# Optimization experiments

Measured on AMD Instinct MI355X. Metric: run time of the kernel, lower is better.

The kernel has to match this reference:

```python
import jax, jax.numpy as jnp
import numpy as np


def setup_inputs() -> dict:
    key = jax.random.key(0)
    k1, = jax.random.split(key, 1)
    B, L, D = 128, 1024, 768
    hidden_states = jax.random.normal(k1, (B, L, D), dtype=jnp.float32)
    attention_mask = jnp.zeros((B, 1, 1, L), dtype=jnp.float32)
    return {"hidden_states": hidden_states, "attention_mask": attention_mask, "K": 512}


def reference(hidden_states, attention_mask, K):
    B, L, D = hidden_states.shape
    # r tokens to merge, protected class token (ToMe: r = min(r, (t - protected)//2))
    r = max(0, L - K)
    r = min(r, (L - 1) // 2)

    # --- bipartite soft matching (indices computed under no_grad in torch) ---
    metric = hidden_states / jnp.linalg.norm(hidden_states, axis=-1, keepdims=True)
    a = metric[:, ::2, :]   # [B, t1, D] even tokens (src side)
    b = metric[:, 1::2, :]  # [B, t2, D] odd tokens (dst side)
    scores = jnp.einsum('bid,bjd->bij', a, b)  # [B, t1, t2]
    scores = scores.at[:, 0, :].set(-jnp.inf)  # protect class token (row 0 of src)
    node_max = jnp.max(scores, axis=-1)        # [B, t1]
    node_idx = jnp.argmax(scores, axis=-1)     # [B, t1] best dst per src
    order = jnp.argsort(-node_max, axis=-1)    # descending similarity
    src_idx = order[:, :r]                     # [B, r] tokens to merge away
    unm_idx = jnp.sort(order[:, r:], axis=-1)  # [B, t1-r] kept src tokens (sorted: class_token=True)
    dst_idx = jnp.take_along_axis(node_idx, src_idx, axis=-1)  # [B, r]

    # --- merge(x, mode='mean') with include_self=True ---
    src = hidden_states[:, ::2, :]   # [B, t1, D]
    dst = hidden_states[:, 1::2, :]  # [B, t2, D]
    t2 = dst.shape[1]
    unm = jnp.take_along_axis(src, unm_idx[..., None], axis=1)     # [B, t1-r, D]
    src_g = jnp.take_along_axis(src, src_idx[..., None], axis=1)   # [B, r, D]
    bidx = jnp.arange(B)[:, None]
    dst_sum = dst.at[bidx, dst_idx].add(src_g)                     # self + merged srcs
    counts = jnp.ones((B, t2), dtype=hidden_states.dtype).at[bidx, dst_idx].add(1.0)
    dst_mean = dst_sum / counts[..., None]

    preserved_tokens = jnp.concatenate([unm, dst_mean], axis=1)    # [B, t1-r+t2, D]
    final_attention_mask = jnp.zeros((B, 1, 1, preserved_tokens.shape[1]),
                                     dtype=hidden_states.dtype)
    return preserved_tokens, final_attention_mask
```

## Files before the change

### kernel.cpp

```cpp
#include <hip/hip_runtime.h>
#include <hip/hip_bf16.h>

#define B_ 128
#define L_ 1024
#define T_ 512
#define D_ 768
#define CH_ 96
#define DT_ 513
#define TAU_C 1e-3f
#define PBUF_ 1024

typedef __attribute__((ext_vector_type(8))) short bf16x8;
typedef __attribute__((ext_vector_type(4))) float f32x4;

typedef const __attribute__((address_space(1))) unsigned int* gas1_t;
typedef __attribute__((address_space(3))) unsigned int* gas3_t;

__device__ __forceinline__ unsigned short f2bf_rne(float x){
    unsigned u = __float_as_uint(x);
    unsigned r = (u + 0x7FFFu + ((u >> 16) & 1u)) >> 16;
    return (unsigned short)r;
}

__global__ __launch_bounds__(256) void pack_k(const float* __restrict__ hs,
                                              unsigned short* __restrict__ Apk,
                                              unsigned short* __restrict__ Bpk,
                                              double* __restrict__ nsq,
                                              int* __restrict__ paircnt){
    __shared__ __align__(16) unsigned short LhS[CH_ * 16 * 8];
    if (blockIdx.x == 0 && threadIdx.x == 0) *paircnt = 0;
    int b = blockIdx.x >> 6, g = blockIdx.x & 63;
    int wv = threadIdx.x >> 6, lane = threadIdx.x & 63;

    #pragma unroll
    for (int rr = 0; rr < 4; ++rr){
        int jj = wv * 4 + rr;
        long seq = (long)b * L_ + g * 16 + jj;
        const float4* src = (const float4*)(hs + seq * D_);
        float4 f0 = src[lane], f1 = src[lane + 64], f2 = src[lane + 128];
        double s = 0.0;
        s += (double)f0.x*f0.x + (double)f0.y*f0.y + (double)f0.z*f0.z + (double)f0.w*f0.w;
        s += (double)f1.x*f1.x + (double)f1.y*f1.y + (double)f1.z*f1.z + (double)f1.w*f1.w;
        s += (double)f2.x*f2.x + (double)f2.y*f2.y + (double)f2.z*f2.z + (double)f2.w*f2.w;
        #pragma unroll
        for (int off = 32; off; off >>= 1) s += __shfl_xor(s, off);
        if (lane == 0 && (jj & 1)) nsq[seq] = s;
        float rn = (float)(1.0 / sqrt(s));
        float4 fv[3] = {f0, f1, f2};
        #pragma unroll
        for (int t = 0; t < 3; ++t){
            int e0 = t * 256 + lane * 4;
            int c = e0 >> 3, ei = e0 & 7;
            float vv[4] = {fv[t].x, fv[t].y, fv[t].z, fv[t].w};
            short4 hv;
            #pragma unroll
            for (int e = 0; e < 4; ++e)
                ((short*)&hv)[e] = (short)f2bf_rne(vv[e] * rn);
            int o = c * 128 + ((jj ^ (c & 7)) << 3) + ei;
            *(short4*)(LhS + o) = hv;
        }
    }
    __syncthreads();
    #pragma unroll
    for (int it = 0; it < 6; ++it){
        int linear = it * 256 + threadIdx.x;
        int c = linear >> 4, jj = linear & 15;
        int o = c * 128 + ((jj ^ (c & 7)) << 3);
        int tok = g * 8 + (jj >> 1);
        long go = ((long)(b * CH_ + c) * T_ + tok) * 8;
        if (jj & 1) *(bf16x8*)(Bpk + go) = *(const bf16x8*)(LhS + o);
        else        *(bf16x8*)(Apk + go) = *(const bf16x8*)(LhS + o);
    }
}

__global__ __launch_bounds__(512, 2) void coarse_k(const unsigned short* __restrict__ Apk,
                                                   const unsigned short* __restrict__ Bpk,
                                                   int* __restrict__ node_idx,
                                                   unsigned long long* __restrict__ rowkey,
                                                   int* __restrict__ paircnt,
                                                   int2* __restrict__ pairs){
    __shared__ __align__(16) unsigned short A_lds[CH_ * 64 * 8];
    __shared__ float pm1s[64][8];
    __shared__ int   pjs [64][8];
    __shared__ float m1f[64];
    __shared__ int   cnd[64];
    __shared__ int2  pbuf[PBUF_];
    __shared__ int   pcnt_s, pbase_s;

    int bid = blockIdx.x;
    int xcd = bid & 7, q = bid >> 3;
    int it = q & 7, bhi = q >> 3;
    int b = xcd + 8 * bhi;

    int tid = threadIdx.x;
    int w = tid >> 6, lane = tid & 63, l15 = lane & 15, l4 = lane >> 4;

    long pkbase = (long)b * CH_ * T_;

    #pragma unroll
    for (int n = 0; n < 12; ++n){
        int c = w * 12 + n;
        const unsigned short* src = Apk + (pkbase + (long)c * T_ + it * 64 + lane) * 8;
        __builtin_amdgcn_global_load_lds((gas1_t)src, (gas3_t)(A_lds + c * 512), 16, 0, 0);
    }

    const unsigned short* pB0 = Bpk + (pkbase + (long)l4 * T_ + w * 64 + l15) * 8;
    const long KSTEP = (long)4 * T_ * 8;

    f32x4 acc[4][4];
    #pragma unroll
    for (int i = 0; i < 4; ++i)
        #pragma unroll
        for (int j = 0; j < 4; ++j) acc[i][j] = (f32x4){0.f, 0.f, 0.f, 0.f};

    bf16x8 bq0[4], bq1[4];
    #pragma unroll
    for (int jb = 0; jb < 4; ++jb){
        bq0[jb] = *(const bf16x8*)(pB0 + 0 * KSTEP + jb * 128);
        bq1[jb] = *(const bf16x8*)(pB0 + 1 * KSTEP + jb * 128);
    }
    __syncthreads();

    if (tid == 0) pcnt_s = 0;

    #pragma unroll
    for (int s = 0; s < 24; ++s){
        bf16x8 bq2[4];
        if (s < 22){
            #pragma unroll
            for (int jb = 0; jb < 4; ++jb)
                bq2[jb] = *(const bf16x8*)(pB0 + (long)(s + 2) * KSTEP + jb * 128);
        }
        bf16x8 ah[4];
        #pragma unroll
        for (int ib = 0; ib < 4; ++ib)
            ah[ib] = *(const bf16x8*)(A_lds + ((s * 4 + l4) * 64 + ib * 16 + l15) * 8);
        if (s & 1){
            #pragma unroll
            for (int jb = 0; jb < 4; ++jb)
                #pragma unroll
                for (int ib = 0; ib < 4; ++ib)
                    acc[ib][jb] = __builtin_amdgcn_mfma_f32_16x16x32_bf16(ah[ib], bq1[jb], acc[ib][jb], 0, 0, 0);
            if (s < 22){
                #pragma unroll
                for (int jb = 0; jb < 4; ++jb) bq1[jb] = bq2[jb];
            }
        } else {
            #pragma unroll
            for (int jb = 0; jb < 4; ++jb)
                #pragma unroll
                for (int ib = 0; ib < 4; ++ib)
                    acc[ib][jb] = __builtin_amdgcn_mfma_f32_16x16x32_bf16(ah[ib], bq0[jb], acc[ib][jb], 0, 0, 0);
            if (s < 22){
                #pragma unroll
                for (int jb = 0; jb < 4; ++jb) bq0[jb] = bq2[jb];
            }
        }
    }

    #pragma unroll
    for (int ib = 0; ib < 4; ++ib)
        #pragma unroll
        for (int rr = 0; rr < 4; ++rr){
            float m1 = -1e30f; int j1 = 0;
            #pragma unroll
            for (int jb = 0; jb < 4; ++jb){
                float v = acc[ib][jb][rr];
                int col = w * 64 + jb * 16 + l15;
                if (v > m1){ m1 = v; j1 = col; }
            }
            #pragma unroll
            for (int m = 1; m < 16; m <<= 1){
                float o1 = __shfl_xor(m1, m);
                int   oj = __shfl_xor(j1, m);
                if (o1 > m1 || (o1 == m1 && oj < j1)){ m1 = o1; j1 = oj; }
            }
            if (l15 == 0){
                int row = ib * 16 + l4 * 4 + rr;
                pm1s[row][w] = m1; pjs[row][w] = j1;
            }
        }
    __syncthreads();
    int grow0 = b * T_ + it * 64;
    if (tid < 64){
        float M1 = -1e30f; int J1 = 0;
        #pragma unroll
        for (int w2 = 0; w2 < 8; ++w2){
            float a1 = pm1s[tid][w2]; int aj = pjs[tid][w2];
            if (a1 > M1){ M1 = a1; J1 = aj; }
        }
        node_idx[grow0 + tid] = J1;
        m1f[tid] = M1;
        cnd[tid] = 0;
        rowkey[grow0 + tid] = 0ULL;
    }
    __syncthreads();
    #pragma unroll
    for (int ib = 0; ib < 4; ++ib)
        #pragma unroll
        for (int rr = 0; rr < 4; ++rr){
            int row = ib * 16 + l4 * 4 + rr;
            float thr_ = m1f[row] - TAU_C;
            int hits = 0;
            #pragma unroll
            for (int jb = 0; jb < 4; ++jb) hits += (acc[ib][jb][rr] > thr_) ? 1 : 0;
            if (hits) atomicAdd(&cnd[row], hits);
        }
    __syncthreads();
    #pragma unroll
    for (int ib = 0; ib < 4; ++ib)
        #pragma unroll
        for (int rr = 0; rr < 4; ++rr){
            int row = ib * 16 + l4 * 4 + rr;
            if (cnd[row] < 2) continue;
            if (it == 0 && row == 0) continue;
            float thr_ = m1f[row] - TAU_C;
            #pragma unroll
            for (int jb = 0; jb < 4; ++jb)
                if (acc[ib][jb][rr] > thr_){
                    int idx = atomicAdd(&pcnt_s, 1);
                    int2 pr = make_int2(grow0 + row, w * 64 + jb * 16 + l15);
                    if (idx < PBUF_) pbuf[idx] = pr;
                    else { int p = atomicAdd(paircnt, 1); pairs[p] = pr; }
                }
        }
    __syncthreads();
    if (tid == 0){
        int n = min(pcnt_s, PBUF_);
        pbase_s = atomicAdd(paircnt, n);
    }
    __syncthreads();
    int n = min(pcnt_s, PBUF_);
    for (int k2 = tid; k2 < n; k2 += 512) pairs[pbase_s + k2] = pbuf[k2];
}

__global__ __launch_bounds__(256) void refine_k(const float* __restrict__ hs,
                                                const double* __restrict__ nsq,
                                                const int* __restrict__ paircnt,
                                                const int2* __restrict__ pairs,
                                                unsigned long long* __restrict__ rowkey){
    int n = *paircnt;
    int w = threadIdx.x >> 6, lane = threadIdx.x & 63;
    for (int p = blockIdx.x * 4 + w; p < n; p += gridDim.x * 4){
        int2 pr = pairs[p];
        int grow = pr.x, j = pr.y;
        int b = grow >> 9, i = grow & 511;
        const float* ar = hs + ((long)b * L_ + 2 * i) * D_;
        const float* br = hs + ((long)b * L_ + 2 * j + 1) * D_;
        double s = 0.0;
        #pragma unroll
        for (int dd = 0; dd < 12; ++dd){
            int d = dd * 64 + lane;
            s += (double)ar[d] * (double)br[d];
        }
        #pragma unroll
        for (int off = 32; off; off >>= 1) s += __shfl_xor(s, off);
        if (lane == 0){
            double sc = s / sqrt(nsq[(long)b * L_ + 2 * j + 1]);
            unsigned long long bits = (unsigned long long)__double_as_longlong(sc);
            unsigned long long key = (bits >> 63) ? ~bits : (bits | 0x8000000000000000ULL);
            key = (key & ~0xFFFFULL) | (unsigned long long)(511 - j);
            atomicMax(&rowkey[grow], key);
        }
    }
}

__global__ __launch_bounds__(512) void csr_k(const int* __restrict__ node_idx,
                                             const unsigned long long* __restrict__ rowkey,
                                             int* __restrict__ goff,
                                             int* __restrict__ glist){
    __shared__ int sidx[512];
    __shared__ int off[513];
    __shared__ int tmp[512];
    __shared__ int cnt[512];
    int b = blockIdx.x, t = threadIdx.x;
    unsigned long long rk = rowkey[b * T_ + t];
    sidx[t] = rk ? (511 - (int)(rk & 0xFFFFULL)) : node_idx[b * T_ + t];
    cnt[t] = 0;
    __syncthreads();
    if (t >= 1) atomicAdd(&cnt[sidx[t]], 1);
    __syncthreads();
    tmp[t] = cnt[t];
    __syncthreads();
    for (int s = 1; s < 512; s <<= 1){
        int v = (t >= s) ? tmp[t - s] : 0;
        __syncthreads();
        tmp[t] += v;
        __syncthreads();
    }
    if (t == 0) off[0] = 0;
    off[t + 1] = tmp[t];
    __syncthreads();
    if (t >= 1){
        int j = sidx[t], r = 0;
        for (int i2 = 1; i2 < t; ++i2) r += (sidx[i2] == j);
        glist[b * T_ + off[j] + r] = t;
    }
    goff[b * 513 + t] = off[t];
    if (t == 0) goff[b * 513 + 512] = off[512];
}

__global__ __launch_bounds__(192) void merge_k(const float* __restrict__ hs,
                                               const int* __restrict__ goff,
                                               const int* __restrict__ glist,
                                               float* __restrict__ out){
    int bid = blockIdx.x;
    int b = bid / DT_, jj = bid - b * DT_;
    long obase4 = ((long)b * DT_ + jj) * (D_ / 4);
    float4* out4 = (float4*)out;
    if (threadIdx.x == 0) out[(long)B_ * DT_ * D_ + b * DT_ + jj] = 0.0f;
    int d = threadIdx.x;
    if (jj == 0){
        const float4* src = (const float4*)(hs + (long)b * L_ * D_);
        out4[obase4 + d] = src[d];
        return;
    }
    int j = jj - 1;
    int o0 = goff[b * 513 + j], o1 = goff[b * 513 + j + 1];
    const float4* dst = (const float4*)(hs + ((long)b * L_ + 2 * j + 1) * D_);
    float4 a = dst[d];
    for (int s = o0; s < o1; ++s){
        int i = glist[b * T_ + s];
        const float4* srow = (const float4*)(hs + ((long)b * L_ + 2 * i) * D_);
        float4 v = srow[d];
        a.x += v.x; a.y += v.y; a.z += v.z; a.w += v.w;
    }
    float rc = 1.0f / (float)(o1 - o0 + 1);
    a.x *= rc; a.y *= rc; a.z *= rc; a.w *= rc;
    out4[obase4 + d] = a;
}

extern "C" void kernel_launch(void* const* d_in, const int* in_sizes, int n_in,
                              void* d_out, int out_size, void* d_ws, size_t ws_size,
                              hipStream_t stream){
    const float* hs = (const float*)d_in[0];
    float* out = (float*)d_out;
    char* ws = (char*)d_ws;

    const long PSZ = (long)B_ * CH_ * T_ * 8;
    unsigned short* Apk = (unsigned short*)ws;
    unsigned short* Bpk = Apk + PSZ;
    double* nsq      = (double*)(ws + 201326592);
    int*    node_idx = (int*)   (ws + 202375168);
    unsigned long long* rowkey = (unsigned long long*)(ws + 202637312);
    int*    paircnt  = (int*)   (ws + 203161600);
    int*    goff     = (int*)   (ws + 203161856);
    int*    glist    = (int*)   (ws + 203425024);
    int2*   pairs    = (int2*)  (ws + 203687168);

    pack_k  <<<B_ * 64, 256, 0, stream>>>(hs, Apk, Bpk, nsq, paircnt);
    coarse_k<<<B_ * 8, 512, 0, stream>>>(Apk, Bpk, node_idx, rowkey, paircnt, pairs);
    refine_k<<<512, 256, 0, stream>>>(hs, nsq, paircnt, pairs, rowkey);
    csr_k   <<<B_, 512, 0, stream>>>(node_idx, rowkey, goff, glist);
    merge_k <<<B_ * DT_, 192, 0, stream>>>(hs, goff, glist, out);
}
```

Before: 391.7 us.

## Stage B operand through triple-buffered LDS with async global-to-LDS loads in coarse GEMM

Reworks the coarse similarity GEMM so B tiles are loaded into a triple-buffered LDS ring with global_load_lds, instead of each wave loading B straight from global into registers. Each k-step is split into two column halves, with prefetch two phases ahead, padded LDS strides to reduce bank conflicts, and raised wave priority around the MFMA bursts. The aim is to share B loads across waves and hide memory latency. The cost is a barrier every phase and a remapped column layout for the argmax and pair-emission code. It also aliases the epilogue scratch onto the same LDS and adds a tie-break in the cross-wave argmax.

```diff
diff --git a/kernel.cpp b/kernel.cpp
--- a/kernel.cpp
+++ b/kernel.cpp
@@ -9,6 +9,13 @@
 #define DT_ 513
 #define TAU_C 1e-3f
 #define PBUF_ 1024
+
+#define A_CSTR 1040
+#define A_BYTES (CH_ * A_CSTR)
+#define B_CSTR 4112
+#define B_BUFB (4 * B_CSTR)
+#define B_OFF A_BYTES
+#define SMEM_BYTES (A_BYTES + 3 * B_BUFB)
 
 typedef __attribute__((ext_vector_type(8))) short bf16x8;
 typedef __attribute__((ext_vector_type(4))) float f32x4;
@@ -79,13 +86,7 @@
                                                    unsigned long long* __restrict__ rowkey,
                                                    int* __restrict__ paircnt,
                                                    int2* __restrict__ pairs){
-    __shared__ __align__(16) unsigned short A_lds[CH_ * 64 * 8];
-    __shared__ float pm1s[64][8];
-    __shared__ int   pjs [64][8];
-    __shared__ float m1f[64];
-    __shared__ int   cnd[64];
-    __shared__ int2  pbuf[PBUF_];
-    __shared__ int   pcnt_s, pbase_s;
+    __shared__ __align__(16) char SMEM[SMEM_BYTES];
 
     int bid = blockIdx.x;
     int xcd = bid & 7, q = bid >> 3;
@@ -101,11 +102,21 @@
     for (int n = 0; n < 12; ++n){
         int c = w * 12 + n;
         const unsigned short* src = Apk + (pkbase + (long)c * T_ + it * 64 + lane) * 8;
-        __builtin_amdgcn_global_load_lds((gas1_t)src, (gas3_t)(A_lds + c * 512), 16, 0, 0);
-    }
-
-    const unsigned short* pB0 = Bpk + (pkbase + (long)l4 * T_ + w * 64 + l15) * 8;
-    const long KSTEP = (long)4 * T_ * 8;
+        __builtin_amdgcn_global_load_lds((gas1_t)src, (gas3_t)(SMEM + c * A_CSTR), 16, 0, 0);
+    }
+    {
+        int qq = w, c_rel = qq >> 2, tblk = qq & 3;
+        #pragma unroll
+        for (int n = 0; n < 2; ++n){
+            int q2 = w + 8 * n, cr = q2 >> 2, tb = q2 & 3;
+            const unsigned short* s0 = Bpk + (pkbase + (long)cr * T_ + 0 * 256 + tb * 64 + lane) * 8;
+            __builtin_amdgcn_global_load_lds((gas1_t)s0, (gas3_t)(SMEM + B_OFF + 0 * B_BUFB + cr * B_CSTR + tb * 1024), 16, 0, 0);
+            const unsigned short* s1 = Bpk + (pkbase + (long)cr * T_ + 1 * 256 + tb * 64 + lane) * 8;
+            __builtin_amdgcn_global_load_lds((gas1_t)s1, (gas3_t)(SMEM + B_OFF + 1 * B_BUFB + cr * B_CSTR + tb * 1024), 16, 0, 0);
+        }
+        (void)qq; (void)c_rel; (void)tblk;
+    }
+    __syncthreads();
 
     f32x4 acc[4][4];
     #pragma unroll
@@ -113,50 +124,50 @@
         #pragma unroll
         for (int j = 0; j < 4; ++j) acc[i][j] = (f32x4){0.f, 0.f, 0.f, 0.f};
 
-    bf16x8 bq0[4], bq1[4];
-    #pragma unroll
-    for (int jb = 0; jb < 4; ++jb){
-        bq0[jb] = *(const bf16x8*)(pB0 + 0 * KSTEP + jb * 128);
-        bq1[jb] = *(const bf16x8*)(pB0 + 1 * KSTEP + jb * 128);
-    }
-    __syncthreads();
-
-    if (tid == 0) pcnt_s = 0;
-
-    #pragma unroll
-    for (int s = 0; s < 24; ++s){
-        bf16x8 bq2[4];
-        if (s < 22){
-            #pragma unroll
-            for (int jb = 0; jb < 4; ++jb)
-                bq2[jb] = *(const bf16x8*)(pB0 + (long)(s + 2) * KSTEP + jb * 128);
-        }
-        bf16x8 ah[4];
-        #pragma unroll
-        for (int ib = 0; ib < 4; ++ib)
-            ah[ib] = *(const bf16x8*)(A_lds + ((s * 4 + l4) * 64 + ib * 16 + l15) * 8);
-        if (s & 1){
-            #pragma unroll
-            for (int jb = 0; jb < 4; ++jb)
-                #pragma unroll
-                for (int ib = 0; ib < 4; ++ib)
-                    acc[ib][jb] = __builtin_amdgcn_mfma_f32_16x16x32_bf16(ah[ib], bq1[jb], acc[ib][jb], 0, 0, 0);
-            if (s < 22){
-                #pragma unroll
-                for (int jb = 0; jb < 4; ++jb) bq1[jb] = bq2[jb];
+    bf16x8 ah[4];
+    #pragma unroll
+    for (int ph = 0; ph < 48; ++ph){
+        int s = ph >> 1, h = ph & 1, buf = ph % 3;
+        if (ph < 46){
+            int sn = (ph + 2) >> 1, hn = (ph + 2) & 1, bn = (ph + 2) % 3;
+            #pragma unroll
+            for (int n = 0; n < 2; ++n){
+                int q2 = w + 8 * n, cr = q2 >> 2, tb = q2 & 3;
+                const unsigned short* src = Bpk + (pkbase + (long)(sn * 4 + cr) * T_ + hn * 256 + tb * 64 + lane) * 8;
+                __builtin_amdgcn_global_load_lds((gas1_t)src, (gas3_t)(SMEM + B_OFF + bn * B_BUFB + cr * B_CSTR + tb * 1024), 16, 0, 0);
             }
-        } else {
-            #pragma unroll
-            for (int jb = 0; jb < 4; ++jb)
-                #pragma unroll
-                for (int ib = 0; ib < 4; ++ib)
-                    acc[ib][jb] = __builtin_amdgcn_mfma_f32_16x16x32_bf16(ah[ib], bq0[jb], acc[ib][jb], 0, 0, 0);
-            if (s < 22){
-                #pragma unroll
-                for (int jb = 0; jb < 4; ++jb) bq0[jb] = bq2[jb];
-            }
-        }
-    }
+        }
+        if (h == 0){
+            #pragma unroll
+            for (int ib = 0; ib < 4; ++ib)
+                ah[ib] = *(const bf16x8*)(SMEM + (s * 4 + l4) * A_CSTR + (ib * 16 + l15) * 16);
+        }
+        bf16x8 bh[2];
+        #pragma unroll
+        for (int g = 0; g < 2; ++g)
+            bh[g] = *(const bf16x8*)(SMEM + B_OFF + buf * B_BUFB + l4 * B_CSTR + (w * 32 + g * 16 + l15) * 16);
+
+        __builtin_amdgcn_s_setprio(1);
+        #pragma unroll
+        for (int g = 0; g < 2; ++g)
+            #pragma unroll
+            for (int ib = 0; ib < 4; ++ib)
+                acc[ib][h * 2 + g] = __builtin_amdgcn_mfma_f32_16x16x32_bf16(ah[ib], bh[g], acc[ib][h * 2 + g], 0, 0, 0);
+        __builtin_amdgcn_s_setprio(0);
+
+        if (ph < 46) asm volatile("s_waitcnt vmcnt(2)" ::: "memory");
+        else         asm volatile("s_waitcnt vmcnt(0)" ::: "memory");
+        __builtin_amdgcn_s_barrier();
+        asm volatile("" ::: "memory");
+    }
+
+    float* pm1s = (float*)SMEM;
+    int*   pjs  = (int*)(SMEM + 2048);
+    float* m1f  = (float*)(SMEM + 4096);
+    int*   cnd  = (int*)(SMEM + 4352);
+    int2*  pbuf = (int2*)(SMEM + 4608);
+    int*   pcnt_s  = (int*)(SMEM + 12800);
+    int*   pbase_s = (int*)(SMEM + 12804);
 
     #pragma unroll
     for (int ib = 0; ib < 4; ++ib)
@@ -164,9 +175,10 @@
         for (int rr = 0; rr < 4; ++rr){
             float m1 = -1e30f; int j1 = 0;
             #pragma unroll
-            for (int jb = 0; jb < 4; ++jb){
+            for (int jb2 = 0; jb2 < 4; ++jb2){
+                int jb = ((jb2 & 1) << 1) | (jb2 >> 1);
                 float v = acc[ib][jb][rr];
-                int col = w * 64 + jb * 16 + l15;
+                int col = (jb >> 1) * 256 + w * 32 + (jb & 1) * 16 + l15;
                 if (v > m1){ m1 = v; j1 = col; }
             }
             #pragma unroll
@@ -177,7 +189,7 @@
             }
             if (l15 == 0){
                 int row = ib * 16 + l4 * 4 + rr;
-                pm1s[row][w] = m1; pjs[row][w] = j1;
+                pm1s[row * 8 + w] = m1; pjs[row * 8 + w] = j1;
             }
         }
     __syncthreads();
@@ -186,13 +198,14 @@
         float M1 = -1e30f; int J1 = 0;
         #pragma unroll
         for (int w2 = 0; w2 < 8; ++w2){
-            float a1 = pm1s[tid][w2]; int aj = pjs[tid][w2];
-            if (a1 > M1){ M1 = a1; J1 = aj; }
+            float a1 = pm1s[tid * 8 + w2]; int aj = pjs[tid * 8 + w2];
+            if (a1 > M1 || (a1 == M1 && aj < J1)){ M1 = a1; J1 = aj; }
         }
         node_idx[grow0 + tid] = J1;
         m1f[tid] = M1;
         cnd[tid] = 0;
         rowkey[grow0 + tid] = 0ULL;
+        if (tid == 0) *pcnt_s = 0;
     }
     __syncthreads();
     #pragma unroll
@@ -218,20 +231,17 @@
             #pragma unroll
             for (int jb = 0; jb < 4; ++jb)
                 if (acc[ib][jb][rr] > thr_){
-                    int idx = atomicAdd(&pcnt_s, 1);
-                    int2 pr = make_int2(grow0 + row, w * 64 + jb * 16 + l15);
+                    int idx = atomicAdd(pcnt_s, 1);
+                    int2 pr = make_int2(grow0 + row, (jb >> 1) * 256 + w * 32 + (jb & 1) * 16 + l15);
                     if (idx < PBUF_) pbuf[idx] = pr;
                     else { int p = atomicAdd(paircnt, 1); pairs[p] = pr; }
                 }
         }
     __syncthreads();
-    if (tid == 0){
-        int n = min(pcnt_s, PBUF_);
-        pbase_s = atomicAdd(paircnt, n);
-    }
-    __syncthreads();
-    int n = min(pcnt_s, PBUF_);
-    for (int k2 = tid; k2 < n; k2 += 512) pairs[pbase_s + k2] = pbuf[k2];
+    if (tid == 0) *pbase_s = atomicAdd(paircnt, min(*pcnt_s, PBUF_));
+    __syncthreads();
+    int n = min(*pcnt_s, PBUF_);
+    for (int k2 = tid; k2 < n; k2 += 512) pairs[*pbase_s + k2] = pbuf[k2];
 }
 
 __global__ __launch_bounds__(256) void refine_k(const float* __restrict__ hs,
```

New measurement: 369.0 us. 1.06x faster.
